# Optimization experiments

Hardware: AMD Instinct MI355X
Metric: run time of the kernel (lower is better)

The kernel has to match this reference:

```python
import jax, jax.numpy as jnp
import numpy as np

K_NEIGHBORS = 3


def setup_inputs() -> dict:
    key = jax.random.key(0)
    k1, k2 = jax.random.split(key)
    B, E, Hl, Wl = 8, 768, 32, 32   # ViT-Base latent grid for 512x512 / patch 16
    N = 20000                        # size of fitted kNN memory bank
    embeddings = jax.random.normal(k1, (B, E, Hl, Wl), dtype=jnp.float32)
    bank = jax.random.normal(k2, (N, E), dtype=jnp.float32)
    return {"embeddings": embeddings, "bank": bank, "out_size": 512}


def reference(embeddings, bank, out_size):
    # embeddings: [B, E, Hl, Wl]; bank: [N, E]
    B, E, Hl, Wl = embeddings.shape
    # permute(0,2,3,1) then flatten H,W -> queries [B, Hl*Wl, E]
    q = jnp.transpose(embeddings, (0, 2, 3, 1)).reshape(B, Hl * Wl, E)
    # squared Euclidean distances via ||q||^2 + ||b||^2 - 2 q.b
    q2 = jnp.sum(q * q, axis=-1, keepdims=True)            # [B, Q, 1]
    b2 = jnp.sum(bank * bank, axis=-1)                      # [N]
    d2 = q2 + b2[None, None, :] - 2.0 * jnp.einsum('bqe,ne->bqn', q, bank)  # [B, Q, N]
    # k nearest = top-k of negated squared distance
    neg_top, _ = jax.lax.top_k(-d2, K_NEIGHBORS)            # [B, Q, K]
    dist = jnp.sqrt(jnp.maximum(-neg_top, 1e-12))           # Euclidean distances
    scores = dist.mean(axis=-1).reshape(B, Hl, Wl)          # mean over k neighbors
    # F.interpolate(..., mode='bilinear') default align_corners=False == half-pixel
    out = jax.image.resize(scores[:, None, :, :], (B, 1, out_size, out_size), method='bilinear')
    return out
```

## Files before the change

kernel.cpp:

```cpp
#include <hip/hip_runtime.h>
#include <math.h>

#define KD     768
#define MT     64
#define NT     128
#define KB     128
#define NKC    6
#define NSPLIT 32
#define BIGF   3.0e38f

typedef __attribute__((ext_vector_type(4))) int   i32x4;
typedef __attribute__((ext_vector_type(8))) int   i32x8;
typedef __attribute__((ext_vector_type(4))) float f32x4;

__device__ __forceinline__ unsigned f2e4m3(float x) {
    unsigned u = __float_as_uint(x);
    unsigned s = (u >> 24) & 0x80u;
    float ax = __uint_as_float(u & 0x7fffffffu);
    if (ax < 0.015625f) {
        int n = (int)rintf(ax * 512.0f);
        if (n >= 8) return s | 0x08u;
        return s | (unsigned)n;
    }
    if (ax >= 464.0f) return s | 0x7Eu;
    unsigned m = __float_as_uint(ax);
    unsigned low = m & 0xFFFFFu;
    unsigned r = m >> 20;
    r += (low > 0x80000u) || (low == 0x80000u && (r & 1u));
    int ef = (int)(r >> 3) - 120;
    return s | ((unsigned)ef << 3) | (r & 7u);
}

__device__ __forceinline__ void ins3(float* t, float v) {
    float lo0 = fminf(t[0], v);
    float hi0 = fmaxf(t[0], v);
    float lo1 = fminf(t[1], hi0);
    float hi1 = fmaxf(t[1], hi0);
    float lo2 = fminf(t[2], hi1);
    t[0] = lo0; t[1] = lo1; t[2] = lo2;
}
__device__ __forceinline__ void async16(unsigned char* lds, const unsigned char* g) {
    __builtin_amdgcn_global_load_lds(
        (const __attribute__((address_space(1))) unsigned int*)g,
        (__attribute__((address_space(3))) unsigned int*)lds, 16, 0, 0);
}

__global__ void q_prep_k(const float* __restrict__ emb, unsigned char* __restrict__ qf8,
                         float* __restrict__ q2) {
    __shared__ float s[64][65];
    int bx  = blockIdx.x;
    int b   = bx / 192;
    int rem = bx % 192;
    int hw0 = (rem & 15) * 64;
    int eg  = rem >> 4;
    int e0  = eg * 64;
    const float* src = emb + (size_t)b * KD * 1024;
    unsigned int* q4 = (unsigned int*)qf8;
    #pragma unroll
    for (int i = 0; i < 16; ++i) {
        int idx = threadIdx.x + i * 256;
        int ee = idx >> 6, hh = idx & 63;
        s[ee][hh] = src[(size_t)(e0 + ee) * 1024 + hw0 + hh];
    }
    __syncthreads();
    #pragma unroll
    for (int i = 0; i < 4; ++i) {
        int slot = threadIdx.x + i * 256;
        int qq = slot >> 4, e4 = slot & 15;
        float v0 = s[e4 * 4 + 0][qq], v1 = s[e4 * 4 + 1][qq];
        float v2 = s[e4 * 4 + 2][qq], v3 = s[e4 * 4 + 3][qq];
        unsigned p = f2e4m3(v0) | (f2e4m3(v1) << 8)
                   | (f2e4m3(v2) << 16) | (f2e4m3(v3) << 24);
        q4[((size_t)b * 1024 + hw0 + qq) * (KD / 4) + e0 / 4 + e4] = p;
        float part = 0.f;
        part = fmaf(v0, v0, part); part = fmaf(v1, v1, part);
        part = fmaf(v2, v2, part); part = fmaf(v3, v3, part);
        #pragma unroll
        for (int off = 1; off < 16; off <<= 1) part += __shfl_xor(part, off, 64);
        if ((threadIdx.x & 15) == 0) atomicAdd(&q2[b * 1024 + hw0 + qq], part);
    }
}

__global__ void bank_prep_k(const float* __restrict__ bank, unsigned char* __restrict__ bf8,
                            float* __restrict__ b2, int N, int Npad) {
    int gid = blockIdx.x * 256 + threadIdx.x;
    int row = gid >> 6, lane = gid & 63;
    if (row >= Npad) return;
    unsigned int* b4 = (unsigned int*)bf8;
    if (row < N) {
        const float4* src = (const float4*)(bank + (size_t)row * KD);
        float s = 0.f;
        #pragma unroll
        for (int i = 0; i < KD / 256; ++i) {
            float4 v = src[lane + i * 64];
            s = fmaf(v.x, v.x, s); s = fmaf(v.y, v.y, s);
            s = fmaf(v.z, v.z, s); s = fmaf(v.w, v.w, s);
            unsigned p = f2e4m3(v.x) | (f2e4m3(v.y) << 8)
                       | (f2e4m3(v.z) << 16) | (f2e4m3(v.w) << 24);
            b4[(size_t)row * (KD / 4) + lane + i * 64] = p;
        }
        #pragma unroll
        for (int off = 32; off; off >>= 1) s += __shfl_down(s, off, 64);
        if (lane == 0) b2[row] = s;
    } else {
        #pragma unroll
        for (int i = 0; i < KD / 256; ++i) b4[(size_t)row * (KD / 4) + lane + i * 64] = 0;
        if (lane == 0) b2[row] = BIGF;
    }
}

__device__ __forceinline__ void stage_w(unsigned char* buf, const unsigned char* gB,
                                        int k0, int tid) {
    #pragma unroll
    for (int h = 0; h < 2; ++h)
        #pragma unroll
        for (int i = 0; i < 4; ++i) {
            int s = tid + i * 256;
            int m = s >> 3, g = s & 7;
            int G = g ^ (m & 7);
            async16(buf + h * (NT * KB) + s * 16,
                    gB + (size_t)m * KD + k0 + h * KB + G * 16);
        }
}

__device__ __forceinline__ i32x8 frag_read(const unsigned char* st, int base, int o0, int o1) {
    i32x4 lo = *(const i32x4*)&st[base + o0];
    i32x4 hi = *(const i32x4*)&st[base + o1];
    return __builtin_shufflevector(lo, hi, 0, 1, 2, 3, 4, 5, 6, 7);
}

__global__ __launch_bounds__(256, 2)
void knn_mfma_k(const unsigned char* __restrict__ qf8, const unsigned char* __restrict__ bf8,
                const float* __restrict__ b2g, float* __restrict__ cand,
                int ntiles, int Q) {
    __shared__ unsigned char bst[2][2 * NT * KB];
    __shared__ float b2s[5 * NT];

    const int tid  = threadIdx.x;
    const int lane = tid & 63;
    const int quad = lane >> 4;
    const int l15  = lane & 15;
    const int wid  = tid >> 6;
    const int wm   = wid & 1;
    const int wn   = wid >> 1;
    const int xr   = l15 & 7;

    const int bx   = blockIdx.x;
    const int xcd  = bx & 7;
    const int rr_  = bx >> 9;
    const int jj   = (bx >> 3) & 63;
    const int mt   = xcd * 16 + (jj & 15);
    const int sp   = (jj >> 4) + 4 * rr_;
    const int Mbase = mt * MT;

    const int numnt = (ntiles - sp + NSPLIT - 1) / NSPLIT;

    for (int idx = tid; idx < numnt * NT; idx += 256) {
        int slot = idx >> 7, col = idx & 127;
        b2s[idx] = b2g[(size_t)(sp + slot * NSPLIT) * NT + col];
    }

    const unsigned char* gA = qf8 + ((size_t)Mbase + 32 * wm + l15) * KD + quad * 32;
    i32x8 af[NKC][2];
    #pragma unroll
    for (int kc = 0; kc < NKC; ++kc)
        #pragma unroll
        for (int mi = 0; mi < 2; ++mi) {
            const i32x4* p = (const i32x4*)(gA + (size_t)mi * 16 * KD + kc * KB);
            i32x4 lo = p[0];
            i32x4 hi = p[1];
            af[kc][mi] = __builtin_shufflevector(lo, hi, 0, 1, 2, 3, 4, 5, 6, 7);
        }

    float top3[24];
    #pragma unroll
    for (int i = 0; i < 24; ++i) top3[i] = BIGF;
    f32x4 acc[2][4];
    #pragma unroll
    for (int a = 0; a < 2; ++a)
        #pragma unroll
        for (int b = 0; b < 4; ++b) acc[a][b] = (f32x4){0.f, 0.f, 0.f, 0.f};

    const int o0 = ((2 * quad) ^ xr) * 16;
    const int o1 = ((2 * quad + 1) ^ xr) * 16;
    int bb[4];
    #pragma unroll
    for (int ni = 0; ni < 4; ++ni) bb[ni] = (64 * wn + 16 * ni + l15) * KB;

    __syncthreads();

    const unsigned char* gB0 = bf8 + (size_t)sp * NT * KD;
    stage_w(bst[0], gB0, 0, tid);

    int pp = 0;
    for (int i = 0; i < numnt; ++i) {
        const unsigned char* gBc = bf8 + (size_t)(sp + i * NSPLIT) * NT * KD;
        const bool lastt = (i == numnt - 1);
        const unsigned char* gBn = lastt ? gBc
                                 : bf8 + (size_t)(sp + (i + 1) * NSPLIT) * NT * KD;
        #pragma unroll
        for (int w = 0; w < 3; ++w) {
            asm volatile("s_waitcnt vmcnt(0)" ::: "memory");
            __builtin_amdgcn_s_barrier();
            if (!(lastt && w == 2)) {
                if (w < 2) stage_w(bst[pp ^ 1], gBc, (2 * w + 2) * KB, tid);
                else       stage_w(bst[pp ^ 1], gBn, 0, tid);
            }
            const unsigned char* st = bst[pp];
            i32x8 ba[4], bbf[4];
            #pragma unroll
            for (int ni = 0; ni < 4; ++ni) ba[ni] = frag_read(st, bb[ni], o0, o1);
            #pragma unroll
            for (int ni = 0; ni < 4; ++ni)
                bbf[ni] = frag_read(st + NT * KB, bb[ni], o0, o1);
            #pragma unroll
            for (int ni = 0; ni < 4; ++ni)
                #pragma unroll
                for (int mi = 0; mi < 2; ++mi)
                    acc[mi][ni] = __builtin_amdgcn_mfma_scale_f32_16x16x128_f8f6f4(
                        af[2 * w][mi], ba[ni], acc[mi][ni], 0, 0,
                        0, 127, 0, 127);
            #pragma unroll
            for (int ni = 0; ni < 4; ++ni)
                #pragma unroll
                for (int mi = 0; mi < 2; ++mi)
                    acc[mi][ni] = __builtin_amdgcn_mfma_scale_f32_16x16x128_f8f6f4(
                        af[2 * w + 1][mi], bbf[ni], acc[mi][ni], 0, 0,
                        0, 127, 0, 127);
            pp ^= 1;
        }
        const float* b2p = &b2s[i * NT + 64 * wn];
        #pragma unroll
        for (int ni = 0; ni < 4; ++ni) {
            float b2v = b2p[16 * ni + l15];
            #pragma unroll
            for (int mi = 0; mi < 2; ++mi)
                #pragma unroll
                for (int r = 0; r < 4; ++r) {
                    float s = fmaf(-2.0f, acc[mi][ni][r], b2v);
                    ins3(&top3[(mi * 4 + r) * 3], s);
                }
        }
        #pragma unroll
        for (int a = 0; a < 2; ++a)
            #pragma unroll
            for (int b = 0; b < 4; ++b) acc[a][b] = (f32x4){0.f, 0.f, 0.f, 0.f};
    }

    #pragma unroll
    for (int mi = 0; mi < 2; ++mi)
        #pragma unroll
        for (int r = 0; r < 4; ++r) {
            float a0 = top3[(mi * 4 + r) * 3 + 0];
            float a1 = top3[(mi * 4 + r) * 3 + 1];
            float a2 = top3[(mi * 4 + r) * 3 + 2];
            #pragma unroll
            for (int off = 1; off < 16; off <<= 1) {
                float b0 = __shfl_xor(a0, off, 64);
                float b1 = __shfl_xor(a1, off, 64);
                float b2x = __shfl_xor(a2, off, 64);
                float t[3] = {a0, a1, a2};
                ins3(t, b0); ins3(t, b1); ins3(t, b2x);
                a0 = t[0]; a1 = t[1]; a2 = t[2];
            }
            if (l15 == 0) {
                int row = Mbase + 32 * wm + 16 * mi + 4 * quad + r;
                float* o = cand + ((size_t)row * 64 + (sp * 2 + wn)) * 3;
                o[0] = a0; o[1] = a1; o[2] = a2;
            }
        }
}

__global__ void scores_k(const float* __restrict__ cand, const float* __restrict__ q2g,
                         float* __restrict__ scores, int Q) {
    int gid  = blockIdx.x * 256 + threadIdx.x;
    int q    = gid >> 6;
    int lane = gid & 63;
    if (q >= Q) return;
    const float* c = cand + ((size_t)q * 64 + lane) * 3;
    float a0 = c[0], a1 = c[1], a2 = c[2];
    #pragma unroll
    for (int off = 1; off < 64; off <<= 1) {
        float b0 = __shfl_xor(a0, off, 64);
        float b1 = __shfl_xor(a1, off, 64);
        float b2x = __shfl_xor(a2, off, 64);
        float t[3] = {a0, a1, a2};
        ins3(t, b0); ins3(t, b1); ins3(t, b2x);
        a0 = t[0]; a1 = t[1]; a2 = t[2];
    }
    if (lane == 0) {
        float q2 = q2g[q];
        float s = (sqrtf(fmaxf(q2 + a0, 1e-12f)) +
                   sqrtf(fmaxf(q2 + a1, 1e-12f)) +
                   sqrtf(fmaxf(q2 + a2, 1e-12f))) * (1.f / 3.f);
        scores[q] = s;
    }
}

__global__ void upsample_k(const float* __restrict__ scores, float* __restrict__ out, int total) {
    int idx = blockIdx.x * blockDim.x + threadIdx.x;
    if (idx >= total) return;
    int x = idx & 511;
    int y = (idx >> 9) & 511;
    int b = idx >> 18;
    float sx = (x + 0.5f) * (1.f / 16.f) - 0.5f;
    float sy = (y + 0.5f) * (1.f / 16.f) - 0.5f;
    int x0 = (int)floorf(sx);
    int y0 = (int)floorf(sy);
    float wx = sx - (float)x0;
    float wy = sy - (float)y0;
    int x0c = min(max(x0, 0), 31), x1c = min(max(x0 + 1, 0), 31);
    int y0c = min(max(y0, 0), 31), y1c = min(max(y0 + 1, 0), 31);
    const float* sb = scores + (size_t)b * 1024;
    float v00 = sb[y0c * 32 + x0c], v01 = sb[y0c * 32 + x1c];
    float v10 = sb[y1c * 32 + x0c], v11 = sb[y1c * 32 + x1c];
    float v0 = v00 + wx * (v01 - v00);
    float v1 = v10 + wx * (v11 - v10);
    out[idx] = v0 + wy * (v1 - v0);
}

extern "C" void kernel_launch(void* const* d_in, const int* in_sizes, int n_in,
                              void* d_out, int out_size, void* d_ws, size_t ws_size,
                              hipStream_t stream) {
    const float* emb  = (const float*)d_in[0];
    const float* bank = (const float*)d_in[1];
    const int Q      = in_sizes[0] / KD;
    const int B      = Q / 1024;
    const int Nbank  = in_sizes[1] / KD;
    const int ntiles = (Nbank + NT - 1) / NT;
    const int Npad   = ntiles * NT;
    const int Mtiles = Q / MT;

    unsigned char* qf8 = (unsigned char*)d_ws;
    unsigned char* bf8 = qf8 + (size_t)Q * KD;
    float* fbase  = (float*)(bf8 + (size_t)Npad * KD);
    float* q2     = fbase;
    float* b2     = q2 + Q;
    float* cand   = b2 + Npad;
    float* scores = cand + (size_t)Q * 64 * 3;
    float* out    = (float*)d_out;

    hipMemsetAsync(q2, 0, Q * sizeof(float), stream);
    hipLaunchKernelGGL(q_prep_k, dim3(B * 192), dim3(256), 0, stream, emb, qf8, q2);
    hipLaunchKernelGGL(bank_prep_k, dim3((Npad * 64 + 255) / 256), dim3(256), 0, stream,
                       bank, bf8, b2, Nbank, Npad);
    hipLaunchKernelGGL(knn_mfma_k, dim3(Mtiles * NSPLIT), dim3(256), 0, stream,
                       qf8, bf8, b2, cand, ntiles, Q);
    hipLaunchKernelGGL(scores_k, dim3((Q * 64 + 255) / 256), dim3(256), 0, stream,
                       cand, q2, scores, Q);
    hipLaunchKernelGGL(upsample_k, dim3((out_size + 255) / 256), dim3(256), 0, stream,
                       scores, out, out_size);
}
```

Measured before the change: 327.9 us.

## Pre-tile FP8 bank in MFMA fragment order for contiguous LDS staging

The bank prep kernel now goes through a shared-memory transpose and writes the FP8 bank in a per-tile, per-k-chunk layout that matches the MFMA fragment order. Each tile's staging becomes a straight contiguous 16-byte async copy, and fragment reads drop the XOR swizzle. The first fragment reads are moved ahead of the next-stage async issue. The cost is a heavier bank prep kernel with one block per tile, a 66KB shared array and 64 strided loads per thread. The unswizzled LDS reads may also hit more bank conflicts.

```diff
diff --git a/kernel.cpp b/kernel.cpp
--- a/kernel.cpp
+++ b/kernel.cpp
@@ -5,6 +5,8 @@
 #define MT     64
 #define NT     128
 #define KB     128
+#define CHK    16384
+#define TILEB  98304
 #define NKC    6
 #define NSPLIT 32
 #define BIGF   3.0e38f
@@ -83,49 +85,64 @@
 
 __global__ void bank_prep_k(const float* __restrict__ bank, unsigned char* __restrict__ bf8,
                             float* __restrict__ b2, int N, int Npad) {
-    int gid = blockIdx.x * 256 + threadIdx.x;
-    int row = gid >> 6, lane = gid & 63;
-    if (row >= Npad) return;
-    unsigned int* b4 = (unsigned int*)bf8;
-    if (row < N) {
-        const float4* src = (const float4*)(bank + (size_t)row * KD);
-        float s = 0.f;
-        #pragma unroll
-        for (int i = 0; i < KD / 256; ++i) {
-            float4 v = src[lane + i * 64];
-            s = fmaf(v.x, v.x, s); s = fmaf(v.y, v.y, s);
-            s = fmaf(v.z, v.z, s); s = fmaf(v.w, v.w, s);
-            unsigned p = f2e4m3(v.x) | (f2e4m3(v.y) << 8)
-                       | (f2e4m3(v.z) << 16) | (f2e4m3(v.w) << 24);
-            b4[(size_t)row * (KD / 4) + lane + i * 64] = p;
-        }
-        #pragma unroll
-        for (int off = 32; off; off >>= 1) s += __shfl_down(s, off, 64);
-        if (lane == 0) b2[row] = s;
-    } else {
-        #pragma unroll
-        for (int i = 0; i < KD / 256; ++i) b4[(size_t)row * (KD / 4) + lane + i * 64] = 0;
-        if (lane == 0) b2[row] = BIGF;
-    }
-}
-
-__device__ __forceinline__ void stage_w(unsigned char* buf, const unsigned char* gB,
-                                        int k0, int tid) {
+    __shared__ float s[128][129];
+    const int tid = threadIdx.x;
+    const int nt  = blockIdx.x;
+    const int r0  = nt * 128;
+    unsigned int* out = (unsigned int*)bf8;
+    const int myrow  = tid >> 1;
+    const int myhalf = tid & 1;
+    float racc = 0.f;
+    for (int kc = 0; kc < NKC; ++kc) {
+        __syncthreads();
+        #pragma unroll
+        for (int i = 0; i < 64; ++i) {
+            int idx = tid + i * 256;
+            int row = idx >> 7, c = idx & 127;
+            int rg = r0 + row;
+            float v = (rg < N) ? bank[(size_t)rg * KD + kc * KB + c] : 0.f;
+            s[row][c] = v;
+        }
+        __syncthreads();
+        #pragma unroll
+        for (int j = 0; j < 64; ++j) {
+            float v = s[myrow][myhalf * 64 + j];
+            racc = fmaf(v, v, racc);
+        }
+        #pragma unroll
+        for (int i = 0; i < 16; ++i) {
+            int d = tid + i * 256;
+            int G = d >> 9, m = (d >> 2) & 127, b4 = d & 3;
+            float f0 = s[m][G * 16 + b4 * 4 + 0];
+            float f1 = s[m][G * 16 + b4 * 4 + 1];
+            float f2 = s[m][G * 16 + b4 * 4 + 2];
+            float f3 = s[m][G * 16 + b4 * 4 + 3];
+            unsigned p = f2e4m3(f0) | (f2e4m3(f1) << 8)
+                       | (f2e4m3(f2) << 16) | (f2e4m3(f3) << 24);
+            out[(size_t)nt * (TILEB / 4) + kc * 4096 + d] = p;
+        }
+    }
+    float pair = racc + __shfl_xor(racc, 1, 64);
+    if (myhalf == 0) {
+        int rg = r0 + myrow;
+        if (rg < Npad) b2[rg] = (rg < N) ? pair : BIGF;
+    }
+}
+
+__device__ __forceinline__ void stage_w(unsigned char* buf, const unsigned char* gT,
+                                        int off, int tid) {
     #pragma unroll
     for (int h = 0; h < 2; ++h)
         #pragma unroll
         for (int i = 0; i < 4; ++i) {
-            int s = tid + i * 256;
-            int m = s >> 3, g = s & 7;
-            int G = g ^ (m & 7);
-            async16(buf + h * (NT * KB) + s * 16,
-                    gB + (size_t)m * KD + k0 + h * KB + G * 16);
-        }
-}
-
-__device__ __forceinline__ i32x8 frag_read(const unsigned char* st, int base, int o0, int o1) {
-    i32x4 lo = *(const i32x4*)&st[base + o0];
-    i32x4 hi = *(const i32x4*)&st[base + o1];
+            int s = (tid + i * 256) * 16;
+            async16(buf + h * CHK + s, gT + off + h * CHK + s);
+        }
+}
+
+__device__ __forceinline__ i32x8 frag_read(const unsigned char* st, int base) {
+    i32x4 lo = *(const i32x4*)&st[base];
+    i32x4 hi = *(const i32x4*)&st[base + 2048];
     return __builtin_shufflevector(lo, hi, 0, 1, 2, 3, 4, 5, 6, 7);
 }
 
@@ -133,7 +150,7 @@
 void knn_mfma_k(const unsigned char* __restrict__ qf8, const unsigned char* __restrict__ bf8,
                 const float* __restrict__ b2g, float* __restrict__ cand,
                 int ntiles, int Q) {
-    __shared__ unsigned char bst[2][2 * NT * KB];
+    __shared__ unsigned char bst[2][2 * CHK];
     __shared__ float b2s[5 * NT];
 
     const int tid  = threadIdx.x;
@@ -143,7 +160,6 @@
     const int wid  = tid >> 6;
     const int wm   = wid & 1;
     const int wn   = wid >> 1;
-    const int xr   = l15 & 7;
 
     const int bx   = blockIdx.x;
     const int xcd  = bx & 7;
@@ -181,38 +197,39 @@
         #pragma unroll
         for (int b = 0; b < 4; ++b) acc[a][b] = (f32x4){0.f, 0.f, 0.f, 0.f};
 
-    const int o0 = ((2 * quad) ^ xr) * 16;
-    const int o1 = ((2 * quad + 1) ^ xr) * 16;
     int bb[4];
     #pragma unroll
-    for (int ni = 0; ni < 4; ++ni) bb[ni] = (64 * wn + 16 * ni + l15) * KB;
+    for (int ni = 0; ni < 4; ++ni)
+        bb[ni] = quad * 4096 + (64 * wn + 16 * ni + l15) * 16 + 256 * 0,
+        bb[ni] = quad * 4096 + 1024 * wn + 256 * ni + 16 * l15;
 
     __syncthreads();
 
-    const unsigned char* gB0 = bf8 + (size_t)sp * NT * KD;
-    stage_w(bst[0], gB0, 0, tid);
+    const unsigned char* gT0 = bf8 + (size_t)sp * TILEB;
+    stage_w(bst[0], gT0, 0, tid);
 
     int pp = 0;
     for (int i = 0; i < numnt; ++i) {
-        const unsigned char* gBc = bf8 + (size_t)(sp + i * NSPLIT) * NT * KD;
+        const unsigned char* gTc = bf8 + (size_t)(sp + i * NSPLIT) * TILEB;
         const bool lastt = (i == numnt - 1);
-        const unsigned char* gBn = lastt ? gBc
-                                 : bf8 + (size_t)(sp + (i + 1) * NSPLIT) * NT * KD;
+        const unsigned char* gTn = lastt ? gTc
+                                 : bf8 + (size_t)(sp + (i + 1) * NSPLIT) * TILEB;
         #pragma unroll
         for (int w = 0; w < 3; ++w) {
             asm volatile("s_waitcnt vmcnt(0)" ::: "memory");
             __builtin_amdgcn_s_barrier();
+            const unsigned char* st = bst[pp];
+            i32x8 ba[4];
+            #pragma unroll
+            for (int ni = 0; ni < 4; ++ni) ba[ni] = frag_read(st, bb[ni]);
             if (!(lastt && w == 2)) {
-                if (w < 2) stage_w(bst[pp ^ 1], gBc, (2 * w + 2) * KB, tid);
-                else       stage_w(bst[pp ^ 1], gBn, 0, tid);
+                if (w < 2) stage_w(bst[pp ^ 1], gTc, (2 * w + 2) * CHK, tid);
+                else       stage_w(bst[pp ^ 1], gTn, 0, tid);
             }
-            const unsigned char* st = bst[pp];
-            i32x8 ba[4], bbf[4];
-            #pragma unroll
-            for (int ni = 0; ni < 4; ++ni) ba[ni] = frag_read(st, bb[ni], o0, o1);
+            i32x8 bbf[4];
             #pragma unroll
             for (int ni = 0; ni < 4; ++ni)
-                bbf[ni] = frag_read(st + NT * KB, bb[ni], o0, o1);
+                bbf[ni] = frag_read(st + CHK, bb[ni]);
             #pragma unroll
             for (int ni = 0; ni < 4; ++ni)
                 #pragma unroll
@@ -342,7 +359,7 @@
 
     hipMemsetAsync(q2, 0, Q * sizeof(float), stream);
     hipLaunchKernelGGL(q_prep_k, dim3(B * 192), dim3(256), 0, stream, emb, qf8, q2);
-    hipLaunchKernelGGL(bank_prep_k, dim3((Npad * 64 + 255) / 256), dim3(256), 0, stream,
+    hipLaunchKernelGGL(bank_prep_k, dim3(ntiles), dim3(256), 0, stream,
                        bank, bf8, b2, Nbank, Npad);
     hipLaunchKernelGGL(knn_mfma_k, dim3(Mtiles * NSPLIT), dim3(256), 0, stream,
                        qf8, bf8, b2, cand, ntiles, Q);
```

Result: slower. 611.9 us (+86.6%).
